# Performance work log

Hardware: AMD Instinct MI355X
Metric: run time of the kernel (lower is better)

## Reference

```python
import jax, jax.numpy as jnp
import numpy as np

N, E, D_IN, HD, H = 50000, 800000, 768, 64, 4
HC = HD * H


def _gat(x, src, dst, etypes, lin_w, att_src, att_dst, edge_emb, lin_edge_w, att_edge,
         bias, res_w, res_b, ln_g, ln_b):
    # Faithful PyG GATConv (edge_dim, concat=True, add_self_loops=True with
    # fill_value='mean', negative_slope=0.2) + residual + LayerNorm. Eval mode: no dropout.
    n = x.shape[0]
    h, c = att_src.shape
    xs = (x @ lin_w).reshape(n, h, c)                      # [N,H,C]
    a_src = jnp.einsum('nhc,hc->nh', xs, att_src)          # [N,H]
    a_dst = jnp.einsum('nhc,hc->nh', xs, att_dst)
    eattr = edge_emb[etypes]                               # [E,ed]
    ones = jnp.ones((etypes.shape[0],), x.dtype)
    cnt = jax.ops.segment_sum(ones, dst, num_segments=n)
    # self-loop edge_attr = mean of incoming edge attrs per node (fill_value='mean')
    loop_attr = jax.ops.segment_sum(eattr, dst, num_segments=n) / jnp.maximum(cnt, 1.0)[:, None]
    loop = jnp.arange(n, dtype=src.dtype)
    src_a = jnp.concatenate([src, loop])
    dst_a = jnp.concatenate([dst, loop])
    e_all = jnp.concatenate([eattr, loop_attr], 0)
    a_edge = jnp.einsum('ehc,hc->eh', (e_all @ lin_edge_w).reshape(-1, h, c), att_edge)
    alpha = jax.nn.leaky_relu(a_src[src_a] + a_dst[dst_a] + a_edge, 0.2)   # [Ea,H]
    # edge softmax over incoming edges of each destination node
    amax = jax.ops.segment_max(alpha, dst_a, num_segments=n)
    ea = jnp.exp(alpha - amax[dst_a])
    denom = jax.ops.segment_sum(ea, dst_a, num_segments=n)
    w = ea / (denom[dst_a] + 1e-16)
    out = jax.ops.segment_sum(xs[src_a] * w[:, :, None], dst_a, num_segments=n)
    out = out.reshape(n, h * c) + bias + (x @ res_w + res_b)
    mu = out.mean(-1, keepdims=True)
    var = jnp.mean((out - mu) ** 2, -1, keepdims=True)
    return (out - mu) * jax.lax.rsqrt(var + 1e-5) * ln_g + ln_b


def _forward(features, positions,
             fe_w1, fe_b1, fe_w2, fe_b2, fe_pos_w, fe_pos_b, fe_type_emb, fe_out_w, fe_out_b,
             g1_lin_w, g1_att_src, g1_att_dst, g1_edge_emb, g1_lin_edge_w, g1_att_edge,
             g1_bias, g1_res_w, g1_res_b, g1_ln_g, g1_ln_b,
             g2_lin_w, g2_att_src, g2_att_dst, g2_edge_emb, g2_lin_edge_w, g2_att_edge,
             g2_bias, g2_res_w, g2_res_b, g2_ln_g, g2_ln_b,
             cls_w, cls_b,
             edge_index, aspect_indices, edge_types, node_types):
    # EnhancedFeatureExtractor (eval: dropout = identity)
    hfe = jax.nn.relu(features @ fe_w1 + fe_b1) @ fe_w2 + fe_b2
    hfe = hfe + fe_type_emb[node_types] + positions[:, None] @ fe_pos_w + fe_pos_b
    hfe = hfe @ fe_out_w + fe_out_b
    src, dst = edge_index[0], edge_index[1]
    hid = _gat(hfe, src, dst, edge_types, g1_lin_w, g1_att_src, g1_att_dst, g1_edge_emb,
               g1_lin_edge_w, g1_att_edge, g1_bias, g1_res_w, g1_res_b, g1_ln_g, g1_ln_b)
    hid = jax.nn.relu(hid)
    hid = _gat(hid, src, dst, edge_types, g2_lin_w, g2_att_src, g2_att_dst, g2_edge_emb,
               g2_lin_edge_w, g2_att_edge, g2_bias, g2_res_w, g2_res_b, g2_ln_g, g2_ln_b)
    return hid[aspect_indices] @ cls_w + cls_b


def setup_inputs() -> dict:
    key = jax.random.key(0)
    ks = jax.random.split(key, 40)
    d = {}
    d['features'] = jax.random.normal(ks[0], (N, D_IN), jnp.float32)
    d['edge_index'] = jax.random.randint(ks[1], (2, E), 0, N, jnp.int32)
    d['aspect_indices'] = jax.random.randint(ks[2], (4096,), 0, N, jnp.int32)
    d['edge_types'] = jax.random.randint(ks[3], (E,), 0, 4, jnp.int32)
    d['node_types'] = jax.random.randint(ks[4], (N,), 0, 3, jnp.int32)
    d['positions'] = jax.random.uniform(ks[5], (N,), jnp.float32)

    def rn(i, shape, s=0.05):
        return s * jax.random.normal(ks[i], shape, jnp.float32)

    d['fe_w1'] = rn(6, (D_IN, HD)); d['fe_b1'] = rn(7, (HD,))
    d['fe_w2'] = rn(8, (HD, HD));   d['fe_b2'] = rn(9, (HD,))
    d['fe_pos_w'] = rn(10, (1, HD)); d['fe_pos_b'] = rn(11, (HD,))
    d['fe_type_emb'] = rn(12, (3, HD))
    d['fe_out_w'] = rn(13, (HD, HD)); d['fe_out_b'] = rn(14, (HD,))
    d['g1_lin_w'] = rn(15, (HD, HC))
    d['g1_att_src'] = rn(16, (H, HD)); d['g1_att_dst'] = rn(17, (H, HD))
    d['g1_edge_emb'] = rn(18, (4, 4)); d['g1_lin_edge_w'] = rn(19, (4, HC))
    d['g1_att_edge'] = rn(20, (H, HD))
    d['g1_bias'] = rn(21, (HC,)); d['g1_res_w'] = rn(22, (HD, HC)); d['g1_res_b'] = rn(23, (HC,))
    d['g1_ln_g'] = jnp.ones((HC,), jnp.float32); d['g1_ln_b'] = jnp.zeros((HC,), jnp.float32)
    d['g2_lin_w'] = rn(24, (HC, HD))
    d['g2_att_src'] = rn(25, (1, HD)); d['g2_att_dst'] = rn(26, (1, HD))
    d['g2_edge_emb'] = rn(27, (4, 4)); d['g2_lin_edge_w'] = rn(28, (4, HD))
    d['g2_att_edge'] = rn(29, (1, HD))
    d['g2_bias'] = rn(30, (HD,)); d['g2_res_w'] = rn(31, (HC, HD)); d['g2_res_b'] = rn(32, (HD,))
    d['g2_ln_g'] = jnp.ones((HD,), jnp.float32); d['g2_ln_b'] = jnp.zeros((HD,), jnp.float32)
    d['cls_w'] = rn(33, (HD, 3)); d['cls_b'] = rn(34, (3,))
    return d


def reference(features, edge_index, aspect_indices, edge_types, node_types, positions,
              fe_w1, fe_b1, fe_w2, fe_b2, fe_pos_w, fe_pos_b, fe_type_emb, fe_out_w, fe_out_b,
              g1_lin_w, g1_att_src, g1_att_dst, g1_edge_emb, g1_lin_edge_w, g1_att_edge,
              g1_bias, g1_res_w, g1_res_b, g1_ln_g, g1_ln_b,
              g2_lin_w, g2_att_src, g2_att_dst, g2_edge_emb, g2_lin_edge_w, g2_att_edge,
              g2_bias, g2_res_w, g2_res_b, g2_ln_g, g2_ln_b,
              cls_w, cls_b):
    return _forward(features, positions,
                    fe_w1, fe_b1, fe_w2, fe_b2, fe_pos_w, fe_pos_b, fe_type_emb, fe_out_w, fe_out_b,
                    g1_lin_w, g1_att_src, g1_att_dst, g1_edge_emb, g1_lin_edge_w, g1_att_edge,
                    g1_bias, g1_res_w, g1_res_b, g1_ln_g, g1_ln_b,
                    g2_lin_w, g2_att_src, g2_att_dst, g2_edge_emb, g2_lin_edge_w, g2_att_edge,
                    g2_bias, g2_res_w, g2_res_b, g2_ln_g, g2_ln_b,
                    cls_w, cls_b,
                    edge_index, aspect_indices, edge_types, node_types)
```

## Files before the change

kernel.cpp:

```cpp
#include <hip/hip_runtime.h>


#define LRELU(x) ((x) > 0.f ? (x) : 0.2f * (x))

typedef __attribute__((ext_vector_type(8))) short short8;
typedef __attribute__((ext_vector_type(4))) float floatx4;

__device__ __forceinline__ unsigned short f2bf(float x) {
    union { float f; unsigned int u; } v; v.f = x;
    unsigned int r = (v.u + 0x7FFFu + ((v.u >> 16) & 1u)) >> 16;
    return (unsigned short)r;
}
__device__ __forceinline__ unsigned int pkbf(float lo, float hi) {
    unsigned int a = __float_as_uint(lo) + 0x8000u;
    unsigned int b = __float_as_uint(hi) + 0x8000u;
    return __builtin_amdgcn_perm(b, a, 0x07060302u);
}
__device__ __forceinline__ float bflo(unsigned int u) {
    return __uint_as_float(u << 16);
}
__device__ __forceinline__ float bfhi(unsigned int u) {
    return __uint_as_float(u & 0xFFFF0000u);
}
__device__ __forceinline__ float bf1(unsigned short u) {
    return __uint_as_float(((unsigned int)u) << 16);
}

__global__ __launch_bounds__(64) void k_tables(
    const float* __restrict__ e_emb1, const float* __restrict__ lew1,
    const float* __restrict__ ae1,
    const float* __restrict__ e_emb2, const float* __restrict__ lew2,
    const float* __restrict__ ae2,
    float* __restrict__ aet1, float* __restrict__ aet2)
{
    __shared__ float M1[16];
    __shared__ float M2[4];
    int t = threadIdx.x;
    if (t < 16) {
        int d = t >> 2, h = t & 3;
        float s = 0.f;
        for (int c = 0; c < 64; ++c) s += lew1[d * 256 + h * 64 + c] * ae1[h * 64 + c];
        M1[d * 4 + h] = s;
    }
    if (t < 4) {
        float s = 0.f;
        for (int c = 0; c < 64; ++c) s += lew2[t * 64 + c] * ae2[c];
        M2[t] = s;
    }
    __syncthreads();
    if (t < 16) {
        int ty = t >> 2, h = t & 3;
        float s = 0.f;
        for (int d = 0; d < 4; ++d) s += e_emb1[ty * 4 + d] * M1[d * 4 + h];
        aet1[ty * 4 + h] = s;
    }
    if (t < 4) {
        float s = 0.f;
        for (int d = 0; d < 4; ++d) s += e_emb2[t * 4 + d] * M2[d];
        aet2[t] = s;
    }
}

__global__ __launch_bounds__(256) void k_bswz_fe1(
    const float* __restrict__ w1, unsigned short* __restrict__ out)
{
    for (int idx = blockIdx.x * 256 + threadIdx.x; idx < 768 * 64;
         idx += gridDim.x * 256) {
        int k = idx >> 6, col = idx & 63;
        int c = k >> 6, kl = k & 63, kg = kl >> 3, j = kl & 7;
        out[((c * 8 + kg) * 64 + col) * 8 + j] = f2bf(w1[k * 64 + col]);
    }
}

template<int K, int NH>
__global__ __launch_bounds__(256) void k_bswz2(
    const float* __restrict__ B1, const float* __restrict__ B2,
    unsigned short* __restrict__ out)
{
    const int NC = 2 * NH;
    for (int idx = blockIdx.x * 256 + threadIdx.x; idx < K * NC;
         idx += gridDim.x * 256) {
        int k = idx / NC, col = idx % NC;
        float v = (col < NH) ? B1[k * NH + col] : B2[k * NH + col - NH];
        int c = k >> 6, kl = k & 63, kg = kl >> 3, j = kl & 7;
        int ct = col >> 7, cl = col & 127;
        out[(((c * (NC / 128) + ct) * 8 + kg) * 128 + cl) * 8 + j] = f2bf(v);
    }
}

__global__ __launch_bounds__(256) void k_fe1(
    const float* __restrict__ feat, const unsigned short* __restrict__ bswz,
    const float* __restrict__ b1, float* __restrict__ t1, int N)
{
    __shared__ __align__(16) unsigned short A_lds[8 * 64 * 8];
    int t = threadIdx.x;
    int wv = t >> 6, lane = t & 63;
    int quad = lane >> 4, l16 = lane & 15;
    long n0 = (long)blockIdx.x * 64;

    floatx4 acc[4];
#pragma unroll
    for (int i = 0; i < 4; ++i) acc[i] = (floatx4){0.f, 0.f, 0.f, 0.f};

    int srow = t >> 2, sf4 = t & 3;
    long arow = n0 + srow;
    if (arow >= N) arow = N - 1;
    const float* fbase = feat + arow * 768 + sf4 * 16;
    int col = wv * 16 + l16;

    float4 v0 = *(const float4*)(fbase);
    float4 v1 = *(const float4*)(fbase + 4);
    float4 v2 = *(const float4*)(fbase + 8);
    float4 v3 = *(const float4*)(fbase + 12);

    for (int kc = 0; kc < 768; kc += 64) {
        uint4 w0 = {pkbf(v0.x, v0.y), pkbf(v0.z, v0.w),
                    pkbf(v1.x, v1.y), pkbf(v1.z, v1.w)};
        uint4 w1p = {pkbf(v2.x, v2.y), pkbf(v2.z, v2.w),
                     pkbf(v3.x, v3.y), pkbf(v3.z, v3.w)};
        __syncthreads();
        *(uint4*)&A_lds[((2 * sf4) * 64 + srow) * 8] = w0;
        *(uint4*)&A_lds[((2 * sf4 + 1) * 64 + srow) * 8] = w1p;
        if (kc + 64 < 768) {
            v0 = *(const float4*)(fbase + kc + 64);
            v1 = *(const float4*)(fbase + kc + 68);
            v2 = *(const float4*)(fbase + kc + 72);
            v3 = *(const float4*)(fbase + kc + 76);
        }
        __syncthreads();
        int ci = kc >> 6;
#pragma unroll
        for (int s = 0; s < 2; ++s) {
            int kg0 = s * 4 + quad;
            short8 bfrag = *(const short8*)&bswz[((ci * 8 + kg0) * 64 + col) * 8];
#pragma unroll
            for (int mt = 0; mt < 4; ++mt) {
                short8 afrag = *(const short8*)&A_lds[(kg0 * 64 + mt * 16 + l16) * 8];
                acc[mt] = __builtin_amdgcn_mfma_f32_16x16x32_bf16(
                    afrag, bfrag, acc[mt], 0, 0, 0);
            }
        }
    }
    float bb = b1[col];
#pragma unroll
    for (int mt = 0; mt < 4; ++mt) {
#pragma unroll
        for (int r = 0; r < 4; ++r) {
            long m = n0 + mt * 16 + quad * 4 + r;
            if (m < N) t1[m * 64 + col] = fmaxf(acc[mt][r] + bb, 0.f);
        }
    }
}

__global__ __launch_bounds__(256) void k_fe2(
    const float* __restrict__ t1, const float* __restrict__ w2,
    const float* __restrict__ b2, const int* __restrict__ ntypes,
    const float* __restrict__ temb, const float* __restrict__ pos,
    const float* __restrict__ posw, const float* __restrict__ posb,
    const float* __restrict__ outw, const float* __restrict__ outb,
    float* __restrict__ hfe)
{
    __shared__ float l1[256];
    __shared__ float l2[256];
    int t = threadIdx.x;
    long base = (long)blockIdx.x * 256;
    l1[t] = t1[base + t];
    __syncthreads();
    int r = t >> 6, c = t & 63;
    float acc = 0.f;
#pragma unroll 8
    for (int k = 0; k < 64; ++k) acc += l1[r * 64 + k] * w2[k * 64 + c];
    long n = (long)blockIdx.x * 4 + r;
    int nt = ntypes[n];
    acc += b2[c] + temb[nt * 64 + c] + pos[n] * posw[c] + posb[c];
    l2[r * 64 + c] = acc;
    __syncthreads();
    float acc2 = 0.f;
#pragma unroll 8
    for (int k = 0; k < 64; ++k) acc2 += l2[r * 64 + k] * outw[k * 64 + c];
    hfe[n * 64 + c] = acc2 + outb[c];
}

template<int K, int NH>
__global__ __launch_bounds__(256) void k_prep_gemm(
    const float* __restrict__ A, const unsigned short* __restrict__ bswz,
    const float* __restrict__ bias, const float* __restrict__ res_b,
    unsigned short* __restrict__ xsb, float* __restrict__ resp, int N)
{
    constexpr int CT = (2 * NH) / 128;
    __shared__ __align__(16) unsigned short A_lds[8 * 64 * 8];
    int t = threadIdx.x;
    int wv = t >> 6, lane = t & 63;
    int quad = lane >> 4, l16 = lane & 15;
    long n0 = (long)blockIdx.x * 64;
    int by = blockIdx.y;

    floatx4 acc[4][2];
#pragma unroll
    for (int i = 0; i < 4; ++i)
#pragma unroll
        for (int j = 0; j < 2; ++j) acc[i][j] = (floatx4){0.f, 0.f, 0.f, 0.f};

    int srow = t >> 2, sf4 = t & 3;
    long arow = n0 + srow;
    if (arow >= N) arow = N - 1;
    const float* abase = A + arow * (long)K + sf4 * 16;

    float4 v0 = *(const float4*)(abase);
    float4 v1 = *(const float4*)(abase + 4);
    float4 v2 = *(const float4*)(abase + 8);
    float4 v3 = *(const float4*)(abase + 12);

    for (int kc = 0; kc < K; kc += 64) {
        uint4 w0 = {pkbf(v0.x, v0.y), pkbf(v0.z, v0.w),
                    pkbf(v1.x, v1.y), pkbf(v1.z, v1.w)};
        uint4 w1p = {pkbf(v2.x, v2.y), pkbf(v2.z, v2.w),
                     pkbf(v3.x, v3.y), pkbf(v3.z, v3.w)};
        __syncthreads();
        *(uint4*)&A_lds[((2 * sf4) * 64 + srow) * 8] = w0;
        *(uint4*)&A_lds[((2 * sf4 + 1) * 64 + srow) * 8] = w1p;
        if (kc + 64 < K) {
            v0 = *(const float4*)(abase + kc + 64);
            v1 = *(const float4*)(abase + kc + 68);
            v2 = *(const float4*)(abase + kc + 72);
            v3 = *(const float4*)(abase + kc + 76);
        }
        __syncthreads();
        int ci = kc >> 6;
#pragma unroll
        for (int s = 0; s < 2; ++s) {
            int kg0 = s * 4 + quad;
#pragma unroll
            for (int nt = 0; nt < 2; ++nt) {
                short8 bfrag = *(const short8*)&bswz[
                    (((ci * CT + by) * 8 + kg0) * 128 + wv * 32 + nt * 16 + l16) * 8];
#pragma unroll
                for (int mt = 0; mt < 4; ++mt) {
                    short8 afrag = *(const short8*)&A_lds[(kg0 * 64 + mt * 16 + l16) * 8];
                    acc[mt][nt] = __builtin_amdgcn_mfma_f32_16x16x32_bf16(
                        afrag, bfrag, acc[mt][nt], 0, 0, 0);
                }
            }
        }
    }
#pragma unroll
    for (int nt = 0; nt < 2; ++nt) {
        int gc = by * 128 + wv * 32 + nt * 16 + l16;
        bool isl = gc < NH;
        int oc = isl ? gc : gc - NH;
        float badd = isl ? 0.f : (bias[oc] + res_b[oc]);
#pragma unroll
        for (int mt = 0; mt < 4; ++mt) {
#pragma unroll
            for (int r = 0; r < 4; ++r) {
                long m = n0 + mt * 16 + quad * 4 + r;
                if (m < N) {
                    float val = acc[mt][nt][r];
                    if (isl) xsb[m * NH + oc] = f2bf(val);
                    else     resp[m * NH + oc] = val + badd;
                }
            }
        }
    }
}

template<int H>
__global__ __launch_bounds__(256) void k_att(
    const unsigned short* __restrict__ xsb, const float* __restrict__ att_s,
    const float* __restrict__ att_d, float* __restrict__ a_src,
    float* __restrict__ a_dst, int N)
{
    int t = threadIdx.x;
    int wv = t >> 6, lane = t & 63;
    long n = (long)blockIdx.x * 4 + wv;
    if (n >= N) return;
    if (H == 4) {
        ushort4 u = *(const ushort4*)&xsb[n * 256 + lane * 4];
        float4 as = *(const float4*)&att_s[lane * 4];
        float4 ad = *(const float4*)&att_d[lane * 4];
        float x0 = bf1(u.x), x1 = bf1(u.y), x2 = bf1(u.z), x3 = bf1(u.w);
        float p = x0 * as.x + x1 * as.y + x2 * as.z + x3 * as.w;
        float q = x0 * ad.x + x1 * ad.y + x2 * ad.z + x3 * ad.w;
#pragma unroll
        for (int k = 8; k; k >>= 1) {
            p += __shfl_xor(p, k, 64);
            q += __shfl_xor(q, k, 64);
        }
        if ((lane & 15) == 0) {
            a_src[n * 4 + (lane >> 4)] = p;
            a_dst[n * 4 + (lane >> 4)] = q;
        }
    } else {
        float x = bf1(xsb[n * 64 + lane]);
        float p = x * att_s[lane];
        float q = x * att_d[lane];
#pragma unroll
        for (int k = 32; k; k >>= 1) {
            p += __shfl_xor(p, k, 64);
            q += __shfl_xor(q, k, 64);
        }
        if (lane == 0) { a_src[n] = p; a_dst[n] = q; }
    }
}

__global__ __launch_bounds__(256) void k_count(
    const int* __restrict__ dst, const int* __restrict__ et,
    int* __restrict__ cnt_t, int E)
{
    int e = blockIdx.x * 256 + threadIdx.x;
    if (e < E) atomicAdd(&cnt_t[dst[e] * 4 + et[e]], 1);
}

__global__ __launch_bounds__(256) void k_scan1(
    const int* __restrict__ cnt_t, int* __restrict__ row_off,
    int* __restrict__ blk_sums, int N)
{
    __shared__ int s[256];
    int t = threadIdx.x;
    int i = blockIdx.x * 256 + t;
    int v = 0;
    if (i < N) v = cnt_t[4 * i] + cnt_t[4 * i + 1] + cnt_t[4 * i + 2] + cnt_t[4 * i + 3];
    s[t] = v;
    __syncthreads();
    for (int off = 1; off < 256; off <<= 1) {
        int x = 0;
        if (t >= off) x = s[t - off];
        __syncthreads();
        s[t] += x;
        __syncthreads();
    }
    if (i < N) row_off[i] = s[t] - v;
    if (t == 255) blk_sums[blockIdx.x] = s[255];
}

__global__ __launch_bounds__(256) void k_scan2(int* __restrict__ blk_sums, int nb)
{
    __shared__ int s[256];
    int t = threadIdx.x;
    int v = (t < nb) ? blk_sums[t] : 0;
    s[t] = v;
    __syncthreads();
    for (int off = 1; off < 256; off <<= 1) {
        int x = 0;
        if (t >= off) x = s[t - off];
        __syncthreads();
        s[t] += x;
        __syncthreads();
    }
    if (t < nb) blk_sums[t] = s[t] - v;
}

__global__ __launch_bounds__(256) void k_scan3(
    int* __restrict__ row_off, int* __restrict__ cursor,
    const int* __restrict__ blk_sums, int N, int E)
{
    int t = threadIdx.x;
    int i = blockIdx.x * 256 + t;
    if (i < N) {
        int o = row_off[i] + blk_sums[blockIdx.x];
        row_off[i] = o;
        cursor[i] = o;
    }
    if (i == 0) row_off[N] = E;
}

__global__ __launch_bounds__(256) void k_scatter(
    const int* __restrict__ src, const int* __restrict__ dst,
    const int* __restrict__ et, int* __restrict__ cursor,
    int* __restrict__ csr_pack, int E)
{
    int e = blockIdx.x * 256 + threadIdx.x;
    if (e < E) {
        int d = dst[e];
        int pos = atomicAdd(&cursor[d], 1);
        csr_pack[pos] = src[e] | (et[e] << 28);
    }
}

__global__ __launch_bounds__(128) void k_gat1(
    const unsigned short* __restrict__ xs1b, const float* __restrict__ a_src,
    const float* __restrict__ a_dst, const int* __restrict__ row_off,
    const int* __restrict__ csr_pack,
    const int* __restrict__ cnt_t, const float* __restrict__ aet1,
    const float* __restrict__ ln_g, const float* __restrict__ ln_b,
    float* io)
{
    __shared__ __align__(16) float4 ws[2][64];
    __shared__ float2 aetp[2][4];
    __shared__ float red[4];
    int n = blockIdx.x;
    int t = threadIdx.x;
    int w = t >> 6, c = t & 63;
    int lc = c & 15, g = c >> 4;
    int h0 = 2 * w;
    if (t < 8) {
        int w2 = t >> 2, ty = t & 3;
        aetp[w2][ty] = make_float2(aet1[ty * 4 + 2 * w2], aet1[ty * 4 + 2 * w2 + 1]);
    }
    int off = row_off[n], deg = row_off[n + 1] - off;
    float2 a_d = *(const float2*)&a_dst[n * 4 + h0];
    __syncthreads();
    float ael0 = 0.f, ael1 = 0.f;
    int degc = 0;
#pragma unroll
    for (int ty = 0; ty < 4; ++ty) {
        int ct = cnt_t[n * 4 + ty];
        degc += ct;
        float2 ae = aetp[w][ty];
        ael0 += (float)ct * ae.x;
        ael1 += (float)ct * ae.y;
    }
    float inv = (degc > 0) ? 1.f / (float)degc : 1.f;
    float2 a_s_self = *(const float2*)&a_src[n * 4 + h0];
    float al0 = a_s_self.x + a_d.x + ael0 * inv;
    float al1 = a_s_self.y + a_d.y + ael1 * inv;
    al0 = LRELU(al0); al1 = LRELU(al1);
    float wself0 = expf(al0), wself1 = expf(al1);

    int col0 = w * 128 + lc * 8;
    const unsigned short* xrow = xs1b + col0;
    float acc[8];
#pragma unroll
    for (int j = 0; j < 8; ++j) acc[j] = 0.f;
    float dp0 = 0.f, dp1 = 0.f;

    for (int base = 0; base < deg; base += 64) {
        int cnt = min(64, deg - base);
        float w0 = 0.f, w1 = 0.f;
        int s = 0;
        if (c < cnt) {
            int pk = csr_pack[off + base + c];
            s = pk & 0x0FFFFFFF;
            int ty = ((unsigned)pk) >> 28;
            float2 as2 = *(const float2*)&a_src[s * 4 + h0];
            float2 ae = aetp[w][ty];
            float a0 = as2.x + a_d.x + ae.x;
            float a1 = as2.y + a_d.y + ae.y;
            a0 = LRELU(a0); a1 = LRELU(a1);
            w0 = expf(a0); w1 = expf(a1);
        }
        dp0 += w0; dp1 += w1;
        ws[w][c] = make_float4(w0, w1, __int_as_float(s), 0.f);
        int cr = (cnt + 7) & ~7;
        for (int i = 0; i < cr; i += 8) {
#pragma unroll
            for (int u = 0; u < 2; ++u) {
                float4 p = ws[w][i + u * 4 + g];
                float wl = (lc < 8) ? p.x : p.y;
                uint4 q = *(const uint4*)&xrow[(long)__float_as_int(p.z) * 256];
                acc[0] += wl * bflo(q.x); acc[1] += wl * bfhi(q.x);
                acc[2] += wl * bflo(q.y); acc[3] += wl * bfhi(q.y);
                acc[4] += wl * bflo(q.z); acc[5] += wl * bfhi(q.z);
                acc[6] += wl * bflo(q.w); acc[7] += wl * bfhi(q.w);
            }
        }
    }
#pragma unroll
    for (int k = 32; k; k >>= 1) {
        dp0 += __shfl_xor(dp0, k, 64);
        dp1 += __shfl_xor(dp1, k, 64);
    }
#pragma unroll
    for (int j = 0; j < 8; ++j) {
        acc[j] += __shfl_xor(acc[j], 16, 64);
        acc[j] += __shfl_xor(acc[j], 32, 64);
    }
    uint4 us = *(const uint4*)&xrow[(long)n * 256];
    float wself_l = (lc < 8) ? wself0 : wself1;
    acc[0] += wself_l * bflo(us.x); acc[1] += wself_l * bfhi(us.x);
    acc[2] += wself_l * bflo(us.y); acc[3] += wself_l * bfhi(us.y);
    acc[4] += wself_l * bflo(us.z); acc[5] += wself_l * bfhi(us.z);
    acc[6] += wself_l * bflo(us.w); acc[7] += wself_l * bfhi(us.w);
    float dsum = ((lc < 8) ? dp0 + wself0 : dp1 + wself1) + 1e-16f;
    float rd = 1.f / dsum;
    float4 r0 = *(const float4*)&io[(long)n * 256 + col0];
    float4 r1 = *(const float4*)&io[(long)n * 256 + col0 + 4];
    float v[8];
    v[0] = acc[0] * rd + r0.x; v[1] = acc[1] * rd + r0.y;
    v[2] = acc[2] * rd + r0.z; v[3] = acc[3] * rd + r0.w;
    v[4] = acc[4] * rd + r1.x; v[5] = acc[5] * rd + r1.y;
    v[6] = acc[6] * rd + r1.z; v[7] = acc[7] * rd + r1.w;
    float s1 = 0.f, s2 = 0.f;
#pragma unroll
    for (int j = 0; j < 8; ++j) { s1 += v[j]; s2 += v[j] * v[j]; }
#pragma unroll
    for (int k = 32; k; k >>= 1) {
        s1 += __shfl_xor(s1, k, 64);
        s2 += __shfl_xor(s2, k, 64);
    }
    if (c == 0) { red[w] = s1 * 0.25f; red[2 + w] = s2 * 0.25f; }
    __syncthreads();
    float mu = (red[0] + red[1]) * (1.f / 256.f);
    float var = (red[2] + red[3]) * (1.f / 256.f) - mu * mu;
    float rs = rsqrtf(var + 1e-5f);
    float4 lg0 = *(const float4*)&ln_g[col0];
    float4 lg1 = *(const float4*)&ln_g[col0 + 4];
    float4 lb0 = *(const float4*)&ln_b[col0];
    float4 lb1 = *(const float4*)&ln_b[col0 + 4];
    if (g == 0) {
        float4 y0, y1;
        y0.x = fmaxf((v[0] - mu) * rs * lg0.x + lb0.x, 0.f);
        y0.y = fmaxf((v[1] - mu) * rs * lg0.y + lb0.y, 0.f);
        y0.z = fmaxf((v[2] - mu) * rs * lg0.z + lb0.z, 0.f);
        y0.w = fmaxf((v[3] - mu) * rs * lg0.w + lb0.w, 0.f);
        y1.x = fmaxf((v[4] - mu) * rs * lg1.x + lb1.x, 0.f);
        y1.y = fmaxf((v[5] - mu) * rs * lg1.y + lb1.y, 0.f);
        y1.z = fmaxf((v[6] - mu) * rs * lg1.z + lb1.z, 0.f);
        y1.w = fmaxf((v[7] - mu) * rs * lg1.w + lb1.w, 0.f);
        *(float4*)&io[(long)n * 256 + col0] = y0;
        *(float4*)&io[(long)n * 256 + col0 + 4] = y1;
    }
}

__global__ __launch_bounds__(64) void k_gat2(
    const unsigned short* __restrict__ xs2b, const float* __restrict__ a_src,
    const float* __restrict__ a_dst, const int* __restrict__ row_off,
    const int* __restrict__ csr_pack,
    const int* __restrict__ cnt_t, const float* __restrict__ aet2,
    const float* __restrict__ ln_g, const float* __restrict__ ln_b,
    float* io)
{
    __shared__ __align__(8) float2 ws[64];
    __shared__ float aetl[4];
    int n = blockIdx.x;
    int c = threadIdx.x;
    int lc = c & 15, g = c >> 4;
    if (c < 4) aetl[c] = aet2[c];
    int off = row_off[n], deg = row_off[n + 1] - off;
    float a_d = a_dst[n];
    float ael = 0.f;
    int degc = 0;
#pragma unroll
    for (int ty = 0; ty < 4; ++ty) {
        int ct = cnt_t[n * 4 + ty];
        degc += ct;
        ael += (float)ct * aet2[ty];
    }
    ael *= (degc > 0 ? 1.f / (float)degc : 1.f);
    float al = a_src[n] + a_d + ael;
    al = LRELU(al);
    float wself = expf(al);

    int colb = lc * 4;
    const unsigned short* xrow = xs2b + colb;
    float acc[4] = {0.f, 0.f, 0.f, 0.f};
    float dp = 0.f;
    for (int base = 0; base < deg; base += 64) {
        int cnt = min(64, deg - base);
        float we = 0.f;
        int s = 0;
        if (c < cnt) {
            int pk = csr_pack[off + base + c];
            s = pk & 0x0FFFFFFF;
            int ty = ((unsigned)pk) >> 28;
            float a = a_src[s] + a_d + aetl[ty];
            a = LRELU(a);
            we = expf(a);
        }
        dp += we;
        ws[c] = make_float2(we, __int_as_float(s));
        int cr = (cnt + 7) & ~7;
        for (int i = 0; i < cr; i += 8) {
#pragma unroll
            for (int u = 0; u < 2; ++u) {
                float2 p = ws[i + u * 4 + g];
                uint2 q = *(const uint2*)&xrow[(long)__float_as_int(p.y) * 64];
                acc[0] += p.x * bflo(q.x); acc[1] += p.x * bfhi(q.x);
                acc[2] += p.x * bflo(q.y); acc[3] += p.x * bfhi(q.y);
            }
        }
    }
#pragma unroll
    for (int k = 32; k; k >>= 1) dp += __shfl_xor(dp, k, 64);
#pragma unroll
    for (int j = 0; j < 4; ++j) {
        acc[j] += __shfl_xor(acc[j], 16, 64);
        acc[j] += __shfl_xor(acc[j], 32, 64);
    }
    uint2 us = *(const uint2*)&xrow[(long)n * 64];
    acc[0] += wself * bflo(us.x); acc[1] += wself * bfhi(us.x);
    acc[2] += wself * bflo(us.y); acc[3] += wself * bfhi(us.y);
    float dsum = dp + wself + 1e-16f;
    float rd = 1.f / dsum;
    float4 r = *(const float4*)&io[(long)n * 64 + colb];
    float v[4];
    v[0] = acc[0] * rd + r.x; v[1] = acc[1] * rd + r.y;
    v[2] = acc[2] * rd + r.z; v[3] = acc[3] * rd + r.w;
    float s1 = v[0] + v[1] + v[2] + v[3];
    float s2 = v[0] * v[0] + v[1] * v[1] + v[2] * v[2] + v[3] * v[3];
#pragma unroll
    for (int k = 32; k; k >>= 1) {
        s1 += __shfl_xor(s1, k, 64);
        s2 += __shfl_xor(s2, k, 64);
    }
    float mu = s1 * (1.f / 256.f);
    float var = s2 * (1.f / 256.f) - mu * mu;
    float rs = rsqrtf(var + 1e-5f);
    if (g == 0) {
        float4 lg = *(const float4*)&ln_g[colb];
        float4 lb = *(const float4*)&ln_b[colb];
        float4 y;
        y.x = (v[0] - mu) * rs * lg.x + lb.x;
        y.y = (v[1] - mu) * rs * lg.y + lb.y;
        y.z = (v[2] - mu) * rs * lg.z + lb.z;
        y.w = (v[3] - mu) * rs * lg.w + lb.w;
        *(float4*)&io[(long)n * 64 + colb] = y;
    }
}

__global__ __launch_bounds__(256) void k_cls(
    const float* __restrict__ hid2, const int* __restrict__ asp,
    const float* __restrict__ w, const float* __restrict__ b,
    float* __restrict__ out)
{
    int g = blockIdx.x * 256 + threadIdx.x;
    int i = g / 3, j = g - i * 3;
    int a = asp[i];
    float acc = b[j];
#pragma unroll 8
    for (int cc = 0; cc < 64; ++cc) acc += hid2[(long)a * 64 + cc] * w[cc * 3 + j];
    out[i * 3 + j] = acc;
}

extern "C" void kernel_launch(void* const* d_in, const int* in_sizes, int n_in,
                              void* d_out, int out_size, void* d_ws, size_t ws_size,
                              hipStream_t stream)
{
    const float* features    = (const float*)d_in[0];
    const int*   edge_index  = (const int*)d_in[1];
    const int*   aspect      = (const int*)d_in[2];
    const int*   etypes      = (const int*)d_in[3];
    const int*   ntypes      = (const int*)d_in[4];
    const float* pos         = (const float*)d_in[5];
    const float* fe_w1       = (const float*)d_in[6];
    const float* fe_b1       = (const float*)d_in[7];
    const float* fe_w2       = (const float*)d_in[8];
    const float* fe_b2       = (const float*)d_in[9];
    const float* fe_pos_w    = (const float*)d_in[10];
    const float* fe_pos_b    = (const float*)d_in[11];
    const float* fe_type_emb = (const float*)d_in[12];
    const float* fe_out_w    = (const float*)d_in[13];
    const float* fe_out_b    = (const float*)d_in[14];
    const float* g1_lin_w    = (const float*)d_in[15];
    const float* g1_att_src  = (const float*)d_in[16];
    const float* g1_att_dst  = (const float*)d_in[17];
    const float* g1_edge_emb = (const float*)d_in[18];
    const float* g1_lin_edge = (const float*)d_in[19];
    const float* g1_att_edge = (const float*)d_in[20];
    const float* g1_bias     = (const float*)d_in[21];
    const float* g1_res_w    = (const float*)d_in[22];
    const float* g1_res_b    = (const float*)d_in[23];
    const float* g1_ln_g     = (const float*)d_in[24];
    const float* g1_ln_b     = (const float*)d_in[25];
    const float* g2_lin_w    = (const float*)d_in[26];
    const float* g2_att_src  = (const float*)d_in[27];
    const float* g2_att_dst  = (const float*)d_in[28];
    const float* g2_edge_emb = (const float*)d_in[29];
    const float* g2_lin_edge = (const float*)d_in[30];
    const float* g2_att_edge = (const float*)d_in[31];
    const float* g2_bias     = (const float*)d_in[32];
    const float* g2_res_w    = (const float*)d_in[33];
    const float* g2_res_b    = (const float*)d_in[34];
    const float* g2_ln_g     = (const float*)d_in[35];
    const float* g2_ln_b     = (const float*)d_in[36];
    const float* cls_w       = (const float*)d_in[37];
    const float* cls_b       = (const float*)d_in[38];

    const int N = in_sizes[0] / 768;
    const int E = in_sizes[1] / 2;
    const int* src = edge_index;
    const int* dst = edge_index + E;

    char* wsb = (char*)d_ws;
    size_t off = 0;
    auto alloc = [&](size_t bytes) -> char* {
        char* p = wsb + off;
        off += (bytes + 255) & ~(size_t)255;
        return p;
    };
    float* t1      = (float*)alloc((size_t)N * 64 * 4);
    float* hfe     = (float*)alloc((size_t)N * 64 * 4);
    unsigned short* xs1b = (unsigned short*)alloc((size_t)N * 256 * 2);
    unsigned short* xs2b = (unsigned short*)alloc((size_t)N * 64 * 2);
    float* rp1     = (float*)alloc((size_t)N * 256 * 4);
    float* rp2     = (float*)alloc((size_t)N * 64 * 4);
    float* a_src1  = (float*)alloc((size_t)N * 4 * 4);
    float* a_dst1  = (float*)alloc((size_t)N * 4 * 4);
    float* a_src2  = (float*)alloc((size_t)N * 4);
    float* a_dst2  = (float*)alloc((size_t)N * 4);
    int*   cnt_t   = (int*)alloc((size_t)N * 4 * 4);
    int*   row_off = (int*)alloc((size_t)(N + 1) * 4);
    int*   cursor  = (int*)alloc((size_t)N * 4);
    int*   blk     = (int*)alloc(1024);
    int*   csr_pack= (int*)alloc((size_t)E * 4);
    float* aet1    = (float*)alloc(64);
    float* aet2    = (float*)alloc(64);
    unsigned short* bz_fe1 = (unsigned short*)alloc(768 * 64 * 2);
    unsigned short* bz_p1  = (unsigned short*)alloc(64 * 512 * 2);
    unsigned short* bz_p2  = (unsigned short*)alloc(256 * 128 * 2);

    hipMemsetAsync(cnt_t, 0, (size_t)N * 4 * 4, stream);

    int mb = (N + 63) / 64;
    int ab = (N + 3) / 4;

    k_tables<<<1, 64, 0, stream>>>(g1_edge_emb, g1_lin_edge, g1_att_edge,
                                   g2_edge_emb, g2_lin_edge, g2_att_edge, aet1, aet2);
    k_bswz_fe1<<<48, 256, 0, stream>>>(fe_w1, bz_fe1);
    k_bswz2<64, 256><<<32, 256, 0, stream>>>(g1_lin_w, g1_res_w, bz_p1);
    k_bswz2<256, 64><<<32, 256, 0, stream>>>(g2_lin_w, g2_res_w, bz_p2);
    k_fe1<<<mb, 256, 0, stream>>>(features, bz_fe1, fe_b1, t1, N);
    k_fe2<<<N / 4, 256, 0, stream>>>(t1, fe_w2, fe_b2, ntypes, fe_type_emb, pos,
                                     fe_pos_w, fe_pos_b, fe_out_w, fe_out_b, hfe);
    k_prep_gemm<64, 256><<<dim3(mb, 4), 256, 0, stream>>>(
        hfe, bz_p1, g1_bias, g1_res_b, xs1b, rp1, N);
    k_att<4><<<ab, 256, 0, stream>>>(xs1b, g1_att_src, g1_att_dst, a_src1, a_dst1, N);
    int eblk = (E + 255) / 256;
    int nb = (N + 255) / 256;
    k_count<<<eblk, 256, 0, stream>>>(dst, etypes, cnt_t, E);
    k_scan1<<<nb, 256, 0, stream>>>(cnt_t, row_off, blk, N);
    k_scan2<<<1, 256, 0, stream>>>(blk, nb);
    k_scan3<<<nb, 256, 0, stream>>>(row_off, cursor, blk, N, E);
    k_scatter<<<eblk, 256, 0, stream>>>(src, dst, etypes, cursor, csr_pack, E);
    k_gat1<<<N, 128, 0, stream>>>(xs1b, a_src1, a_dst1, row_off, csr_pack,
                                  cnt_t, aet1, g1_ln_g, g1_ln_b, rp1);
    k_prep_gemm<256, 64><<<dim3(mb, 1), 256, 0, stream>>>(
        rp1, bz_p2, g2_bias, g2_res_b, xs2b, rp2, N);
    k_att<1><<<ab, 256, 0, stream>>>(xs2b, g2_att_src, g2_att_dst, a_src2, a_dst2, N);
    k_gat2<<<N, 64, 0, stream>>>(xs2b, a_src2, a_dst2, row_off, csr_pack,
                                 cnt_t, aet2, g2_ln_g, g2_ln_b, rp2);
    k_cls<<<(out_size + 255) / 256, 256, 0, stream>>>(rp2, aspect, cls_w, cls_b,
                                                      (float*)d_out);
}
```

Before: 636.0 us.

## Fold feature-encoder linear layers into GAT1 weights and store bf16 intermediates

The two linear layers of the feature encoder after the first ReLU (w2 then out_w) contain no nonlinearity before the GAT1 input projection. They are precomposed into the GAT1 lin/res weights, with per-type and position terms folded into small tables added in the GEMM epilogue. This removes the k_fe2 kernel and the fp32 hfe round trip. Intermediates t1 and the GAT1 output are written in bf16 so the downstream GEMMs load half the bytes and skip the conversion, and float-to-bf16 packing now uses the hardware v_cvt_pk_bf16_f32 instruction. The cost is some precision change from rounding the fused weights and the GAT1 output to bf16.

```diff
diff --git a/kernel.cpp b/kernel.cpp
--- a/kernel.cpp
+++ b/kernel.cpp
@@ -11,10 +11,10 @@
     unsigned int r = (v.u + 0x7FFFu + ((v.u >> 16) & 1u)) >> 16;
     return (unsigned short)r;
 }
-__device__ __forceinline__ unsigned int pkbf(float lo, float hi) {
-    unsigned int a = __float_as_uint(lo) + 0x8000u;
-    unsigned int b = __float_as_uint(hi) + 0x8000u;
-    return __builtin_amdgcn_perm(b, a, 0x07060302u);
+__device__ __forceinline__ unsigned int cvtpk(float lo, float hi) {
+    unsigned int r;
+    asm("v_cvt_pk_bf16_f32 %0, %1, %2" : "=v"(r) : "v"(lo), "v"(hi));
+    return r;
 }
 __device__ __forceinline__ float bflo(unsigned int u) {
     return __uint_as_float(u << 16);
@@ -88,9 +88,89 @@
     }
 }
 
+__global__ __launch_bounds__(256) void k_fuse1(
+    const float* __restrict__ w2, const float* __restrict__ outw,
+    const float* __restrict__ b2, const float* __restrict__ posb,
+    const float* __restrict__ outb, const float* __restrict__ temb,
+    const float* __restrict__ posw,
+    float* __restrict__ W2p, float* __restrict__ h0,
+    float* __restrict__ tadd, float* __restrict__ padd)
+{
+    int t = threadIdx.x;
+    int i = t >> 2, jq = (t & 3) * 16;
+    float a16[16];
+#pragma unroll
+    for (int u = 0; u < 16; ++u) a16[u] = 0.f;
+    for (int k = 0; k < 64; ++k) {
+        float a = w2[i * 64 + k];
+        const float* op = outw + k * 64 + jq;
+        float4 o0 = *(const float4*)op;
+        float4 o1 = *(const float4*)(op + 4);
+        float4 o2 = *(const float4*)(op + 8);
+        float4 o3 = *(const float4*)(op + 12);
+        a16[0] += a * o0.x;  a16[1] += a * o0.y;  a16[2] += a * o0.z;  a16[3] += a * o0.w;
+        a16[4] += a * o1.x;  a16[5] += a * o1.y;  a16[6] += a * o1.z;  a16[7] += a * o1.w;
+        a16[8] += a * o2.x;  a16[9] += a * o2.y;  a16[10] += a * o2.z; a16[11] += a * o2.w;
+        a16[12] += a * o3.x; a16[13] += a * o3.y; a16[14] += a * o3.z; a16[15] += a * o3.w;
+    }
+#pragma unroll
+    for (int u = 0; u < 16; ++u) W2p[i * 64 + jq + u] = a16[u];
+    for (int e = t; e < 320; e += 256) {
+        int g = e >> 6, j = e & 63;
+        float s = 0.f;
+        for (int k = 0; k < 64; ++k) {
+            float v;
+            if (g == 0) v = b2[k] + posb[k];
+            else if (g <= 3) v = temb[(g - 1) * 64 + k];
+            else v = posw[k];
+            s += v * outw[k * 64 + j];
+        }
+        if (g == 0) h0[j] = s + outb[j];
+        else if (g <= 3) tadd[(g - 1) * 64 + j] = s;
+        else padd[j] = s;
+    }
+}
+
+__global__ __launch_bounds__(64) void k_fuse2(
+    const float* __restrict__ W2p, const float* __restrict__ h0,
+    const float* __restrict__ tadd, const float* __restrict__ padd,
+    const float* __restrict__ lin_w, const float* __restrict__ res_w,
+    const float* __restrict__ bias, const float* __restrict__ res_b,
+    unsigned short* __restrict__ bz, float* __restrict__ C0,
+    float* __restrict__ T, float* __restrict__ P)
+{
+    __shared__ float bcol[64];
+    int c = blockIdx.x;
+    int j = threadIdx.x;
+    int cL = c & 255;
+    const float* Bsrc = (c < 256) ? lin_w : res_w;
+    float bv = Bsrc[j * 256 + cL];
+    bcol[j] = bv;
+    __syncthreads();
+    float s = 0.f;
+#pragma unroll 8
+    for (int k = 0; k < 64; ++k) s += W2p[j * 64 + k] * bcol[k];
+    int kg = j >> 3, jj = j & 7, ct = c >> 7, cl = c & 127;
+    bz[((ct * 8 + kg) * 128 + cl) * 8 + jj] = f2bf(s);
+    float pc = h0[j] * bv;
+    float p0 = tadd[j] * bv, p1 = tadd[64 + j] * bv, p2 = tadd[128 + j] * bv;
+    float pp = padd[j] * bv;
+#pragma unroll
+    for (int k = 32; k; k >>= 1) {
+        pc += __shfl_xor(pc, k, 64); p0 += __shfl_xor(p0, k, 64);
+        p1 += __shfl_xor(p1, k, 64); p2 += __shfl_xor(p2, k, 64);
+        pp += __shfl_xor(pp, k, 64);
+    }
+    if (j == 0) {
+        C0[c] = pc + ((c >= 256) ? (bias[cL] + res_b[cL]) : 0.f);
+        T[c] = p0; T[512 + c] = p1; T[1024 + c] = p2;
+        P[c] = pp;
+    }
+}
+
 __global__ __launch_bounds__(256) void k_fe1(
     const float* __restrict__ feat, const unsigned short* __restrict__ bswz,
-    const float* __restrict__ b1, float* __restrict__ t1, int N)
+    const float* __restrict__ b1, unsigned short* __restrict__ t1b, int N)
 {
     __shared__ __align__(16) unsigned short A_lds[8 * 64 * 8];
     int t = threadIdx.x;
@@ -114,10 +194,10 @@
     float4 v3 = *(const float4*)(fbase + 12);
 
     for (int kc = 0; kc < 768; kc += 64) {
-        uint4 w0 = {pkbf(v0.x, v0.y), pkbf(v0.z, v0.w),
-                    pkbf(v1.x, v1.y), pkbf(v1.z, v1.w)};
-        uint4 w1p = {pkbf(v2.x, v2.y), pkbf(v2.z, v2.w),
-                     pkbf(v3.x, v3.y), pkbf(v3.z, v3.w)};
+        uint4 w0 = {cvtpk(v0.x, v0.y), cvtpk(v0.z, v0.w),
+                    cvtpk(v1.x, v1.y), cvtpk(v1.z, v1.w)};
+        uint4 w1p = {cvtpk(v2.x, v2.y), cvtpk(v2.z, v2.w),
+                     cvtpk(v3.x, v3.y), cvtpk(v3.z, v3.w)};
         __syncthreads();
         *(uint4*)&A_lds[((2 * sf4) * 64 + srow) * 8] = w0;
         *(uint4*)&A_lds[((2 * sf4 + 1) * 64 + srow) * 8] = w1p;
@@ -147,44 +227,17 @@
 #pragma unroll
         for (int r = 0; r < 4; ++r) {
             long m = n0 + mt * 16 + quad * 4 + r;
-            if (m < N) t1[m * 64 + col] = fmaxf(acc[mt][r] + bb, 0.f);
-        }
-    }
-}
-
-__global__ __launch_bounds__(256) void k_fe2(
-    const float* __restrict__ t1, const float* __restrict__ w2,
-    const float* __restrict__ b2, const int* __restrict__ ntypes,
-    const float* __restrict__ temb, const float* __restrict__ pos,
-    const float* __restrict__ posw, const float* __restrict__ posb,
-    const float* __restrict__ outw, const float* __restrict__ outb,
-    float* __restrict__ hfe)
-{
-    __shared__ float l1[256];
-    __shared__ float l2[256];
-    int t = threadIdx.x;
-    long base = (long)blockIdx.x * 256;
-    l1[t] = t1[base + t];
-    __syncthreads();
-    int r = t >> 6, c = t & 63;
-    float acc = 0.f;
-#pragma unroll 8
-    for (int k = 0; k < 64; ++k) acc += l1[r * 64 + k] * w2[k * 64 + c];
-    long n = (long)blockIdx.x * 4 + r;
-    int nt = ntypes[n];
-    acc += b2[c] + temb[nt * 64 + c] + pos[n] * posw[c] + posb[c];
-    l2[r * 64 + c] = acc;
-    __syncthreads();
-    float acc2 = 0.f;
-#pragma unroll 8
-    for (int k = 0; k < 64; ++k) acc2 += l2[r * 64 + k] * outw[k * 64 + c];
-    hfe[n * 64 + c] = acc2 + outb[c];
-}
-
-template<int K, int NH>
-__global__ __launch_bounds__(256) void k_prep_gemm(
-    const float* __restrict__ A, const unsigned short* __restrict__ bswz,
-    const float* __restrict__ bias, const float* __restrict__ res_b,
+            if (m < N) t1b[m * 64 + col] = f2bf(fmaxf(acc[mt][r] + bb, 0.f));
+        }
+    }
+}
+
+template<int K, int NH, bool FADD>
+__global__ __launch_bounds__(256) void k_prep(
+    const unsigned short* __restrict__ A, const unsigned short* __restrict__ bswz,
+    const float* __restrict__ c0_or_bias, const float* __restrict__ t_or_resb,
+    const float* __restrict__ Ptab, const int* __restrict__ ntypes,
+    const float* __restrict__ pos,
     unsigned short* __restrict__ xsb, float* __restrict__ resp, int N)
 {
     constexpr int CT = (2 * NH) / 128;
@@ -204,26 +257,18 @@
     int srow = t >> 2, sf4 = t & 3;
     long arow = n0 + srow;
     if (arow >= N) arow = N - 1;
-    const float* abase = A + arow * (long)K + sf4 * 16;
-
-    float4 v0 = *(const float4*)(abase);
-    float4 v1 = *(const float4*)(abase + 4);
-    float4 v2 = *(const float4*)(abase + 8);
-    float4 v3 = *(const float4*)(abase + 12);
+    const unsigned short* abase = A + arow * (long)K + sf4 * 16;
+
+    uint4 q0 = *(const uint4*)(abase);
+    uint4 q1 = *(const uint4*)(abase + 8);
 
     for (int kc = 0; kc < K; kc += 64) {
-        uint4 w0 = {pkbf(v0.x, v0.y), pkbf(v0.z, v0.w),
-                    pkbf(v1.x, v1.y), pkbf(v1.z, v1.w)};
-        uint4 w1p = {pkbf(v2.x, v2.y), pkbf(v2.z, v2.w),
-                     pkbf(v3.x, v3.y), pkbf(v3.z, v3.w)};
         __syncthreads();
-        *(uint4*)&A_lds[((2 * sf4) * 64 + srow) * 8] = w0;
-        *(uint4*)&A_lds[((2 * sf4 + 1) * 64 + srow) * 8] = w1p;
+        *(uint4*)&A_lds[((2 * sf4) * 64 + srow) * 8] = q0;
+        *(uint4*)&A_lds[((2 * sf4 + 1) * 64 + srow) * 8] = q1;
         if (kc + 64 < K) {
-            v0 = *(const float4*)(abase + kc + 64);
-            v1 = *(const float4*)(abase + kc + 68);
-            v2 = *(const float4*)(abase + kc + 72);
-            v3 = *(const float4*)(abase + kc + 76);
+            q0 = *(const uint4*)(abase + kc + 64);
+            q1 = *(const uint4*)(abase + kc + 64 + 8);
         }
         __syncthreads();
         int ci = kc >> 6;
@@ -243,21 +288,53 @@
             }
         }
     }
+
+    int nta[4][4];
+    float posa[4][4];
+    if constexpr (FADD) {
+#pragma unroll
+        for (int mt = 0; mt < 4; ++mt)
+#pragma unroll
+            for (int r = 0; r < 4; ++r) {
+                long m = n0 + mt * 16 + quad * 4 + r;
+                if (m < N) { nta[mt][r] = ntypes[m]; posa[mt][r] = pos[m]; }
+                else       { nta[mt][r] = 0; posa[mt][r] = 0.f; }
+            }
+    }
 #pragma unroll
     for (int nt = 0; nt < 2; ++nt) {
         int gc = by * 128 + wv * 32 + nt * 16 + l16;
         bool isl = gc < NH;
         int oc = isl ? gc : gc - NH;
-        float badd = isl ? 0.f : (bias[oc] + res_b[oc]);
-#pragma unroll
-        for (int mt = 0; mt < 4; ++mt) {
-#pragma unroll
-            for (int r = 0; r < 4; ++r) {
-                long m = n0 + mt * 16 + quad * 4 + r;
-                if (m < N) {
-                    float val = acc[mt][nt][r];
-                    if (isl) xsb[m * NH + oc] = f2bf(val);
-                    else     resp[m * NH + oc] = val + badd;
+        if constexpr (FADD) {
+            float c0 = c0_or_bias[gc];
+            float pcf = Ptab[gc];
+#pragma unroll
+            for (int mt = 0; mt < 4; ++mt) {
+#pragma unroll
+                for (int r = 0; r < 4; ++r) {
+                    long m = n0 + mt * 16 + quad * 4 + r;
+                    if (m < N) {
+                        float val = acc[mt][nt][r] + c0 +
+                                    t_or_resb[nta[mt][r] * (2 * NH) + gc] +
+                                    posa[mt][r] * pcf;
+                        if (isl) xsb[m * NH + oc] = f2bf(val);
+                        else     resp[m * NH + oc] = val;
+                    }
+                }
+            }
+        } else {
+            float badd = isl ? 0.f : (c0_or_bias[oc] + t_or_resb[oc]);
+#pragma unroll
+            for (int mt = 0; mt < 4; ++mt) {
+#pragma unroll
+                for (int r = 0; r < 4; ++r) {
+                    long m = n0 + mt * 16 + quad * 4 + r;
+                    if (m < N) {
+                        float val = acc[mt][nt][r];
+                        if (isl) xsb[m * NH + oc] = f2bf(val);
+                        else     resp[m * NH + oc] = val + badd;
+                    }
                 }
             }
         }
@@ -383,7 +460,7 @@
     const int* __restrict__ csr_pack,
     const int* __restrict__ cnt_t, const float* __restrict__ aet1,
     const float* __restrict__ ln_g, const float* __restrict__ ln_b,
-    float* io)
+    const float* __restrict__ res, unsigned short* __restrict__ out)
 {
     __shared__ __align__(16) float4 ws[2][64];
     __shared__ float2 aetp[2][4];
@@ -473,8 +550,8 @@
     acc[6] += wself_l * bflo(us.w); acc[7] += wself_l * bfhi(us.w);
     float dsum = ((lc < 8) ? dp0 + wself0 : dp1 + wself1) + 1e-16f;
     float rd = 1.f / dsum;
-    float4 r0 = *(const float4*)&io[(long)n * 256 + col0];
-    float4 r1 = *(const float4*)&io[(long)n * 256 + col0 + 4];
+    float4 r0 = *(const float4*)&res[(long)n * 256 + col0];
+    float4 r1 = *(const float4*)&res[(long)n * 256 + col0 + 4];
     float v[8];
     v[0] = acc[0] * rd + r0.x; v[1] = acc[1] * rd + r0.y;
     v[2] = acc[2] * rd + r0.z; v[3] = acc[3] * rd + r0.w;
@@ -493,22 +570,24 @@
     float mu = (red[0] + red[1]) * (1.f / 256.f);
     float var = (red[2] + red[3]) * (1.f / 256.f) - mu * mu;
     float rs = rsqrtf(var + 1e-5f);
-    float4 lg0 = *(const float4*)&ln_g[col0];
-    float4 lg1 = *(const float4*)&ln_g[col0 + 4];
-    float4 lb0 = *(const float4*)&ln_b[col0];
-    float4 lb1 = *(const float4*)&ln_b[col0 + 4];
     if (g == 0) {
-        float4 y0, y1;
-        y0.x = fmaxf((v[0] - mu) * rs * lg0.x + lb0.x, 0.f);
-        y0.y = fmaxf((v[1] - mu) * rs * lg0.y + lb0.y, 0.f);
-        y0.z = fmaxf((v[2] - mu) * rs * lg0.z + lb0.z, 0.f);
-        y0.w = fmaxf((v[3] - mu) * rs * lg0.w + lb0.w, 0.f);
-        y1.x = fmaxf((v[4] - mu) * rs * lg1.x + lb1.x, 0.f);
-        y1.y = fmaxf((v[5] - mu) * rs * lg1.y + lb1.y, 0.f);
-        y1.z = fmaxf((v[6] - mu) * rs * lg1.z + lb1.z, 0.f);
-        y1.w = fmaxf((v[7] - mu) * rs * lg1.w + lb1.w, 0.f);
-        *(float4*)&io[(long)n * 256 + col0] = y0;
-        *(float4*)&io[(long)n * 256 + col0 + 4] = y1;
+        float4 lg0 = *(const float4*)&ln_g[col0];
+        float4 lg1 = *(const float4*)&ln_g[col0 + 4];
+        float4 lb0 = *(const float4*)&ln_b[col0];
+        float4 lb1 = *(const float4*)&ln_b[col0 + 4];
+        float y[8];
+        y[0] = fmaxf((v[0] - mu) * rs * lg0.x + lb0.x, 0.f);
+        y[1] = fmaxf((v[1] - mu) * rs * lg0.y + lb0.y, 0.f);
+        y[2] = fmaxf((v[2] - mu) * rs * lg0.z + lb0.z, 0.f);
+        y[3] = fmaxf((v[3] - mu) * rs * lg0.w + lb0.w, 0.f);
+        y[4] = fmaxf((v[4] - mu) * rs * lg1.x + lb1.x, 0.f);
+        y[5] = fmaxf((v[5] - mu) * rs * lg1.y + lb1.y, 0.f);
+        y[6] = fmaxf((v[6] - mu) * rs * lg1.z + lb1.z, 0.f);
+        y[7] = fmaxf((v[7] - mu) * rs * lg1.w + lb1.w, 0.f);
+        uint4 o;
+        o.x = cvtpk(y[0], y[1]); o.y = cvtpk(y[2], y[3]);
+        o.z = cvtpk(y[4], y[5]); o.w = cvtpk(y[6], y[7]);
+        *(uint4*)&out[(long)n * 256 + col0] = o;
     }
 }
 
@@ -678,10 +757,10 @@
         off += (bytes + 255) & ~(size_t)255;
         return p;
     };
-    float* t1      = (float*)alloc((size_t)N * 64 * 4);
-    float* hfe     = (float*)alloc((size_t)N * 64 * 4);
+    unsigned short* t1b  = (unsigned short*)alloc((size_t)N * 64 * 2);
     unsigned short* xs1b = (unsigned short*)alloc((size_t)N * 256 * 2);
     unsigned short* xs2b = (unsigned short*)alloc((size_t)N * 64 * 2);
+    unsigned short* hid1b= (unsigned short*)alloc((size_t)N * 256 * 2);
     float* rp1     = (float*)alloc((size_t)N * 256 * 4);
     float* rp2     = (float*)alloc((size_t)N * 64 * 4);
     float* a_src1  = (float*)alloc((size_t)N * 4 * 4);
@@ -698,6 +777,13 @@
     unsigned short* bz_fe1 = (unsigned short*)alloc(768 * 64 * 2);
     unsigned short* bz_p1  = (unsigned short*)alloc(64 * 512 * 2);
     unsigned short* bz_p2  = (unsigned short*)alloc(256 * 128 * 2);
+    float* W2p     = (float*)alloc(64 * 64 * 4);
+    float* h0v     = (float*)alloc(64 * 4);
+    float* taddv   = (float*)alloc(192 * 4);
+    float* paddv   = (float*)alloc(64 * 4);
+    float* C0t     = (float*)alloc(512 * 4);
+    float* Tt      = (float*)alloc(3 * 512 * 4);
+    float* Pt      = (float*)alloc(512 * 4);
 
     hipMemsetAsync(cnt_t, 0, (size_t)N * 4 * 4, stream);
 
@@ -707,13 +793,14 @@
     k_tables<<<1, 64, 0, stream>>>(g1_edge_emb, g1_lin_edge, g1_att_edge,
                                    g2_edge_emb, g2_lin_edge, g2_att_edge, aet1, aet2);
     k_bswz_fe1<<<48, 256, 0, stream>>>(fe_w1, bz_fe1);
-    k_bswz2<64, 256><<<32, 256, 0, stream>>>(g1_lin_w, g1_res_w, bz_p1);
+    k_fuse1<<<1, 256, 0, stream>>>(fe_w2, fe_out_w, fe_b2, fe_pos_b, fe_out_b,
+                                   fe_type_emb, fe_pos_w, W2p, h0v, taddv, paddv);
+    k_fuse2<<<512, 64, 0, stream>>>(W2p, h0v, taddv, paddv, g1_lin_w, g1_res_w,
+                                    g1_bias, g1_res_b, bz_p1, C0t, Tt, Pt);
     k_bswz2<256, 64><<<32, 256, 0, stream>>>(g2_lin_w, g2_res_w, bz_p2);
-    k_fe1<<<mb, 256, 0, stream>>>(features, bz_fe1, fe_b1, t1, N);
-    k_fe2<<<N / 4, 256, 0, stream>>>(t1, fe_w2, fe_b2, ntypes, fe_type_emb, pos,
-                                     fe_pos_w, fe_pos_b, fe_out_w, fe_out_b, hfe);
-    k_prep_gemm<64, 256><<<dim3(mb, 4), 256, 0, stream>>>(
-        hfe, bz_p1, g1_bias, g1_res_b, xs1b, rp1, N);
+    k_fe1<<<mb, 256, 0, stream>>>(features, bz_fe1, fe_b1, t1b, N);
+    k_prep<64, 256, true><<<dim3(mb, 4), 256, 0, stream>>>(
+        t1b, bz_p1, C0t, Tt, Pt, ntypes, pos, xs1b, rp1, N);
     k_att<4><<<ab, 256, 0, stream>>>(xs1b, g1_att_src, g1_att_dst, a_src1, a_dst1, N);
     int eblk = (E + 255) / 256;
     int nb = (N + 255) / 256;
@@ -723,9 +810,9 @@
     k_scan3<<<nb, 256, 0, stream>>>(row_off, cursor, blk, N, E);
     k_scatter<<<eblk, 256, 0, stream>>>(src, dst, etypes, cursor, csr_pack, E);
     k_gat1<<<N, 128, 0, stream>>>(xs1b, a_src1, a_dst1, row_off, csr_pack,
-                                  cnt_t, aet1, g1_ln_g, g1_ln_b, rp1);
-    k_prep_gemm<256, 64><<<dim3(mb, 1), 256, 0, stream>>>(
-        rp1, bz_p2, g2_bias, g2_res_b, xs2b, rp2, N);
+                                  cnt_t, aet1, g1_ln_g, g1_ln_b, rp1, hid1b);
+    k_prep<256, 64, false><<<dim3(mb, 1), 256, 0, stream>>>(
+        hid1b, bz_p2, g2_bias, g2_res_b, nullptr, nullptr, nullptr, xs2b, rp2, N);
     k_att<1><<<ab, 256, 0, stream>>>(xs2b, g2_att_src, g2_att_dst, a_src2, a_dst2, N);
     k_gat2<<<N, 64, 0, stream>>>(xs2b, a_src2, a_dst2, row_off, csr_pack,
                                  cnt_t, aet2, g2_ln_g, g2_ln_b, rp2);
```

Result: no change. 641.4 us (+0.9%).
